# Kernel optimization log

Measured on AMD Instinct MI355X. Metric: run time of the kernel, lower is better.

## Reference

```python
import jax, jax.numpy as jnp
import numpy as np

N = 8192
EMB = 256
KDIM = 32
AR = 1024
UTYPE = 233
TEMP = 0.8


def setup_inputs() -> dict:
    key = jax.random.key(0)
    ks = jax.random.split(key, 16)
    s = 0.05
    f32 = jnp.float32
    inp = {
        'utype_mask': jax.random.uniform(ks[0], (UTYPE,), f32),
        'entity_mask': jnp.ones((N,), f32),
        'entity_encodings': jax.random.normal(ks[1], (N, EMB), f32),
        'autoregressive_encoding': jax.random.normal(ks[2], (AR,), f32),
        # func_embed: Linear(233,256)+ReLU
        'W_fe': jax.random.normal(ks[3], (EMB, UTYPE), f32) * s, 'b_fe': jnp.zeros((EMB,), f32),
        # entity_keys: Conv1d(256,32,1) == pointwise linear
        'W_k': jax.random.normal(ks[4], (KDIM, EMB), f32) * s, 'b_k': jnp.zeros((KDIM,), f32),
        # argenc[0]: Linear(1024,256)
        'W_a0': jax.random.normal(ks[5], (EMB, AR), f32) * s, 'b_a0': jnp.zeros((EMB,), f32),
        # argenc[1]: ReLU -> Linear(256,32) -> ReLU
        'W_a1': jax.random.normal(ks[6], (KDIM, EMB), f32) * s, 'b_a1': jnp.zeros((KDIM,), f32),
        # LSTM(64,32) gates (forget, input-sigmoid, input-tanh, output) + shared LayerNorm(32)
        'W_f': jax.random.normal(ks[7], (KDIM, 2 * KDIM), f32) * s, 'b_f': jnp.zeros((KDIM,), f32),
        'W_i0': jax.random.normal(ks[8], (KDIM, 2 * KDIM), f32) * s, 'b_i0': jnp.zeros((KDIM,), f32),
        'W_i1': jax.random.normal(ks[9], (KDIM, 2 * KDIM), f32) * s, 'b_i1': jnp.zeros((KDIM,), f32),
        'W_o': jax.random.normal(ks[10], (KDIM, 2 * KDIM), f32) * s, 'b_o': jnp.zeros((KDIM,), f32),
        'ln_g': jnp.ones((KDIM,), f32), 'ln_b': jnp.zeros((KDIM,), f32),
        # argenc[3]: Linear(32,1024)+ReLU
        'W_a3': jax.random.normal(ks[11], (AR, KDIM), f32) * s, 'b_a3': jnp.zeros((AR,), f32),
        'self_unit_ct': 64,
    }
    return inp


def reference(utype_mask, entity_mask, entity_encodings, autoregressive_encoding,
              W_fe, b_fe, W_k, b_k, W_a0, b_a0, W_a1, b_a1,
              W_f, b_f, W_i0, b_i0, W_i1, b_i1, W_o, b_o, ln_g, ln_b,
              W_a3, b_a3, self_unit_ct):
    n = entity_encodings.shape[0]
    steps = min(64, int(self_unit_ct))

    def ln(x):  # shared LayerNorm(32), torch eps=1e-5, biased var
        m = x.mean()
        v = ((x - m) ** 2).mean()
        return (x - m) * jax.lax.rsqrt(v + 1e-5) * ln_g + ln_b

    def lstm(x, h):
        forget = ln(jax.nn.sigmoid(W_f @ x + b_f))
        remember = ln(jax.nn.sigmoid(W_i0 @ x + b_i0) * jnp.tanh(W_i1 @ x + b_i1))
        new_h = remember + forget * h
        out = jnp.tanh(new_h) * ln(jax.nn.sigmoid(W_o @ x + b_o))
        return out, new_h

    func_embed = jax.nn.relu(W_fe @ utype_mask + b_fe)          # (256,)
    keys = W_k @ entity_encodings.T + b_k[:, None]               # (32, N)

    def step(carry, _):
        q, h, mask, ar, sel, done = carry
        active = jnp.logical_not(done)
        i0 = W_a0 @ ar + b_a0 + func_embed                       # (256,)
        i1 = jax.nn.relu(W_a1 @ jax.nn.relu(i0) + b_a1)          # (32,)
        qn, hn = lstm(jnp.concatenate([i1, q]), h)
        sig = jax.nn.sigmoid(qn @ keys)                          # (N,)
        v = jnp.nan_to_num(jnp.exp(jnp.log(sig) / TEMP))
        ssum = v.sum()
        valid = ssum != 0
        soft = jnp.where(valid, v / jnp.where(valid, ssum, 1.0), 0.0)
        row = jnp.where(active & valid, soft, 0.0)
        pick = jnp.argmax(soft)                                  # deterministic stand-in for multinomial sample
        hit = active & valid & (mask[pick] != 0)
        selection = keys[:, pick]
        centered = selection - selection.mean()
        nan_free = jnp.logical_not(jnp.any(jnp.isnan(centered)))
        mask = jnp.where(hit, mask.at[pick].set(0.0), mask)
        sel = jnp.where(hit, sel.at[pick].set(1.0), sel)
        ar = jnp.where(hit & nan_free, ar + jax.nn.relu(W_a3 @ centered + b_a3), ar)
        done = done | (hit & jnp.logical_not(nan_free))          # emulates break
        q = jnp.where(active, qn, q)
        h = jnp.where(active, hn, h)
        return (q, h, mask, ar, sel, done), row

    init = (jnp.zeros((KDIM,), jnp.float32), jnp.zeros((KDIM,), jnp.float32),
            entity_mask, autoregressive_encoding,
            jnp.zeros((n,), jnp.float32), jnp.array(False))
    (_, _, _, ar_out, sel_out, _), rows = jax.lax.scan(step, init, None, length=steps)
    unit_logits = jnp.zeros((n, n), jnp.float32).at[:steps].set(rows)
    return unit_logits, sel_out, ar_out
```

## Files before the change

kernel.cpp:

```cpp
#include <hip/hip_runtime.h>
#include <math.h>


typedef float v4f __attribute__((ext_vector_type(4)));
typedef unsigned long long ull;

#define N_ENT 8192
#define EMB   256
#define KD    32
#define ARD   1024
#define UT    233
#define NSCAN 32
#define NZERO 224
#define NBLK  256

#define WS_KEYS 0
#define WS_C0   262144
#define WS_PAIR 262400
#define PR_RI0W  0
#define PR_CRI0  512
#define PR_CPART 577
#define PR_KMAX  641
#define PR_SACC  705
#define NPAIRS   737

struct Params {
  const float *um, *emask, *enc, *arin, *W_fe, *b_fe, *W_k, *b_k,
              *W_a0, *b_a0, *W_a1, *b_a1, *W_f, *b_f, *W_i0, *b_i0,
              *W_i1, *b_i1, *W_o, *b_o, *ln_g, *ln_b, *W_a3, *b_a3;
  const int* ct;
  float* out;
  float* wsf;
  int*   wsi;
};

__device__ __forceinline__ ull ld_pair(ull* p_) {
  return __hip_atomic_load(p_, __ATOMIC_RELAXED, __HIP_MEMORY_SCOPE_AGENT);
}
__device__ __forceinline__ void st_pair(ull* p_, ull v) {
  __hip_atomic_store(p_, v, __ATOMIC_RELAXED, __HIP_MEMORY_SCOPE_AGENT);
}
__device__ __forceinline__ void wait_ctr(ull* c, ull target) {
  int guard = 0;
  while (__hip_atomic_load(c, __ATOMIC_RELAXED, __HIP_MEMORY_SCOPE_AGENT) < target) {
    __builtin_amdgcn_s_sleep(1);
    if (++guard > (1 << 20)) break;
  }
}

__global__ __launch_bounds__(256) void k_init(Params p) {
  __shared__ float enc_s[32 * 260];
  __shared__ float um_s[UT];
  const int tid = threadIdx.x, bid = blockIdx.x;
  float* keys = p.wsf + WS_KEYS;

  if (bid == 0 && tid < UT) um_s[tid] = p.um[tid];
  if (bid == 3) {
    ull* pr = (ull*)(p.wsf + WS_PAIR);
    for (int i = tid; i < NPAIRS; i += 256) pr[i] = 0ull;
  }

  const int j0 = bid * 32;
  #pragma unroll
  for (int i = 0; i < 8; ++i) {
    int idx = i * 256 + tid;
    int row = idx >> 6, c4 = idx & 63;
    v4f v = *(const v4f*)(p.enc + (size_t)(j0 + row) * EMB + c4 * 4);
    *(v4f*)&enc_s[row * 260 + c4 * 4] = v;
  }
  __syncthreads();
  {
    const int jl = tid >> 3, kg = tid & 7;
    float acc[4];
    #pragma unroll
    for (int kk = 0; kk < 4; ++kk) acc[kk] = p.b_k[kg * 4 + kk];
    for (int e4 = 0; e4 < 64; ++e4) {
      v4f x = *(const v4f*)&enc_s[jl * 260 + e4 * 4];
      #pragma unroll
      for (int kk = 0; kk < 4; ++kk) {
        v4f w = *(const v4f*)(p.W_k + (size_t)(kg * 4 + kk) * EMB + e4 * 4);
        acc[kk] += x.x * w.x + x.y * w.y + x.z * w.z + x.w * w.w;
      }
    }
    const int j = j0 + jl;
    #pragma unroll
    for (int kk = 0; kk < 4; ++kk) keys[(size_t)(kg * 4 + kk) * N_ENT + j] = acc[kk];
  }
  if (bid == 0) {
    float a = p.b_fe[tid];
    const float* wr = p.W_fe + (size_t)tid * UT;
    for (int u = 0; u < UT; ++u) a += wr[u] * um_s[u];
    p.wsf[WS_C0 + tid] = fmaxf(a, 0.f) + p.b_a0[tid];
  }
}

__global__ __launch_bounds__(256, 1) void k_scan(Params p) {
  const int tid = threadIdx.x, bid = blockIdx.x;
  int ctv = p.ct[0];
  const int steps = ctv < 0 ? 0 : (ctv > 64 ? 64 : ctv);
  const size_t NN = (size_t)N_ENT * N_ENT;

  if (bid >= NSCAN) {
    v4f z = (v4f){0.f, 0.f, 0.f, 0.f};
    v4f* o4 = (v4f*)p.out;
    const size_t tot = NN / 4;
    for (size_t i = (size_t)steps * (N_ENT / 4) + (size_t)(bid - NSCAN) * 256 + tid;
         i < tot; i += (size_t)NZERO * 256)
      __builtin_nontemporal_store(z, o4 + i);
    return;
  }

  __shared__ float ar_s[32 * 33];
  __shared__ float ri0_s[8 * 33];
  __shared__ unsigned maskb[256], selb[256];
  __shared__ float x_i1[32], q_s[32], h_s[32], qnf[32];
  __shared__ float garr[128], fog[32], rem[32], og[32], cent[32];
  __shared__ float b_a1s[32], gb_s[128], lng_s[32], lnb_s[32], c0own[8];
  __shared__ float reds[4], rmaxs[4];
  __shared__ int   ridxs[4];
  __shared__ float ssum_s;
  __shared__ int   upd_s, done_s;

  ull*   pairb = (ull*)(p.wsf + WS_PAIR);
  ull*   ri0w  = pairb + PR_RI0W;
  ull*   cri0  = pairb + PR_CRI0;
  ull*   cpart = pairb + PR_CPART;
  ull*   kmaxp = pairb + PR_KMAX;
  float* saccp = (float*)(pairb + PR_SACC);
  const float* keys = p.wsf + WS_KEYS;

  for (int i = tid; i < ARD; i += 256) ar_s[(i >> 5) * 33 + (i & 31)] = p.arin[i];
  {
    unsigned mb = 0u;
    const float* em = p.emask + (size_t)tid * 32;
    #pragma unroll
    for (int j = 0; j < 32; ++j) mb |= (em[j] != 0.f) ? (1u << j) : 0u;
    maskb[tid] = mb; selb[tid] = 0u;
  }
  if (tid < 32) {
    b_a1s[tid] = p.b_a1[tid];
    lng_s[tid] = p.ln_g[tid]; lnb_s[tid] = p.ln_b[tid];
    q_s[tid] = 0.f; h_s[tid] = 0.f; qnf[tid] = 0.f; x_i1[tid] = 0.f;
  }
  if (tid < 128) {
    const int g = tid >> 5, r = tid & 31;
    const float* bg = (g == 0) ? p.b_f : (g == 1) ? p.b_i0 : (g == 2) ? p.b_i1 : p.b_o;
    gb_s[tid] = bg[r];
  }
  if (tid < 8) c0own[tid] = p.wsf[WS_C0 + bid * 8 + tid];
  if (tid == 0) done_s = 0;

  v4f w0[8];
  { const float* s = p.W_a0 + (size_t)(bid * 8 + (tid >> 5)) * ARD + (tid & 31) * 32;
    #pragma unroll
    for (int i = 0; i < 8; ++i) w0[i] = ((const v4f*)s)[i]; }
  v4f w1[8];
  { const float* s = p.W_a1 + (size_t)(tid >> 3) * EMB + (tid & 7) * 32;
    #pragma unroll
    for (int i = 0; i < 8; ++i) w1[i] = ((const v4f*)s)[i]; }
  v4f wg[8];
  { const int rowg = tid >> 1, g = rowg >> 5, r = rowg & 31, half = tid & 1;
    const float* W = (g == 0) ? p.W_f : (g == 1) ? p.W_i0 : (g == 2) ? p.W_i1 : p.W_o;
    const float* s = W + r * 64 + half * 32;
    #pragma unroll
    for (int i = 0; i < 8; ++i) wg[i] = ((const v4f*)s)[i]; }
  float kc[32];
  { const int gcol = bid * 256 + tid;
    #pragma unroll
    for (int k = 0; k < 32; ++k) kc[k] = keys[(size_t)k * N_ENT + gcol]; }
  __syncthreads();

  auto produce = [&](int tt) {
    const int seg = tid & 31, rl = tid >> 5;
    const float* a = &ar_s[seg * 33];
    float pa = 0.f;
    #pragma unroll
    for (int i = 0; i < 8; ++i) {
      v4f av = *(const v4f*)(a + 4 * i);
      pa += w0[i].x * av.x + w0[i].y * av.y + w0[i].z * av.z + w0[i].w * av.w;
    }
    #pragma unroll
    for (int m = 16; m; m >>= 1) pa += __shfl_xor(pa, m);
    if (seg == 0)
      st_pair(&ri0w[(tt & 1) * 256 + bid * 8 + rl],
              (ull)__float_as_uint(fmaxf(pa + c0own[rl], 0.f)));
  };
  produce(0);
  __syncthreads();
  if (tid == 0)
    __hip_atomic_fetch_add(&cri0[0], 1ull, __ATOMIC_RELAXED, __HIP_MEMORY_SCOPE_AGENT);

  float v_reg = 0.f;
  for (int t = 0; t < steps; ++t) {
    if (tid == 0) wait_ctr(&cri0[t], (ull)NSCAN);
    __syncthreads();
    {
      ull u = ld_pair(&ri0w[(t & 1) * 256 + tid]);
      ri0_s[(tid >> 5) * 33 + (tid & 31)] = __uint_as_float((unsigned)u);
    }
    __syncthreads();
    const int act = (done_s == 0);
    {
      const int r = tid >> 3, s8 = tid & 7;
      float p1 = 0.f;
      #pragma unroll
      for (int i = 0; i < 8; ++i) {
        const float* xx = &ri0_s[s8 * 33 + 4 * i];
        p1 += w1[i].x * xx[0] + w1[i].y * xx[1] + w1[i].z * xx[2] + w1[i].w * xx[3];
      }
      #pragma unroll
      for (int m = 4; m; m >>= 1) p1 += __shfl_xor(p1, m);
      if (s8 == 0) x_i1[r] = fmaxf(p1 + b_a1s[r], 0.f);
    }
    __syncthreads();
    {
      const int rowg = tid >> 1, g = rowg >> 5, half = tid & 1;
      const float* xsrc = half ? q_s : x_i1;
      float pg = 0.f;
      #pragma unroll
      for (int i = 0; i < 8; ++i)
        pg += wg[i].x * xsrc[4 * i] + wg[i].y * xsrc[4 * i + 1] +
              wg[i].z * xsrc[4 * i + 2] + wg[i].w * xsrc[4 * i + 3];
      pg += __shfl_xor(pg, 1);
      if (!half) {
        pg += gb_s[rowg];
        garr[rowg] = (g == 2) ? tanhf(pg) : 1.f / (1.f + __expf(-pg));
      }
    }
    __syncthreads();
    {
      const int w = tid >> 6, k = tid & 63;
      if (w < 3 && k < 32) {
        float a = (w == 0) ? garr[k] : (w == 1) ? garr[32 + k] * garr[64 + k] : garr[96 + k];
        float s = a;
        #pragma unroll
        for (int m = 16; m; m >>= 1) s += __shfl_xor(s, m);
        const float mean = s * (1.f / 32.f);
        const float d = a - mean;
        float vv = d * d;
        #pragma unroll
        for (int m = 16; m; m >>= 1) vv += __shfl_xor(vv, m);
        vv *= (1.f / 32.f);
        const float y = d * rsqrtf(vv + 1e-5f) * lng_s[k] + lnb_s[k];
        if (w == 0) fog[k] = y; else if (w == 1) rem[k] = y; else og[k] = y;
      }
    }
    __syncthreads();
    if (tid < 32) {
      const float nh = rem[tid] + fog[tid] * h_s[tid];
      const float qv = tanhf(nh) * og[tid];
      qnf[tid] = qv;
      if (act) { h_s[tid] = nh; q_s[tid] = qv; }
    }
    __syncthreads();

    {
      float dot = 0.f;
      #pragma unroll
      for (int k = 0; k < 32; ++k) dot += qnf[k] * kc[k];
      const float sig = 1.f / (1.f + __expf(-dot));
      const float v = __expf(__logf(sig) / 0.8f);
      v_reg = v;
      float sv = v, mv = v;
      int mi = (bid << 8) + tid;
      #pragma unroll
      for (int m = 32; m; m >>= 1) {
        sv += __shfl_xor(sv, m);
        const float ov = __shfl_xor(mv, m);
        const int oi = __shfl_xor(mi, m);
        if (ov > mv || (ov == mv && oi < mi)) { mv = ov; mi = oi; }
      }
      const int wv = tid >> 6;
      if ((tid & 63) == 0) { reds[wv] = sv; rmaxs[wv] = mv; ridxs[wv] = mi; }
    }
    __syncthreads();
    if (tid == 0) {
      float Sb = ((reds[0] + reds[1]) + reds[2]) + reds[3];
      float Mb = rmaxs[0]; int Ib = ridxs[0];
      #pragma unroll
      for (int i2 = 1; i2 < 4; ++i2)
        if (rmaxs[i2] > Mb || (rmaxs[i2] == Mb && ridxs[i2] < Ib)) { Mb = rmaxs[i2]; Ib = ridxs[i2]; }
      __hip_atomic_fetch_add(&saccp[t], Sb, __ATOMIC_RELAXED, __HIP_MEMORY_SCOPE_AGENT);
      const ull key = ((ull)__float_as_uint(Mb) << 32) | (ull)(0xFFFFFFFFu - (unsigned)Ib);
      __hip_atomic_fetch_max(&kmaxp[t], key, __ATOMIC_RELAXED, __HIP_MEMORY_SCOPE_AGENT);
      asm volatile("s_waitcnt vmcnt(0)" ::: "memory");
      __hip_atomic_fetch_add(&cpart[t], 1ull, __ATOMIC_RELAXED, __HIP_MEMORY_SCOPE_AGENT);
    }

    if (tid == 0) wait_ctr(&cpart[t], (ull)NSCAN);
    __syncthreads();
    if (tid < 32) {
      const float s = __hip_atomic_load(&saccp[t], __ATOMIC_RELAXED, __HIP_MEMORY_SCOPE_AGENT);
      const ull km = ld_pair(&kmaxp[t]);
      const int ii = (int)(0xFFFFFFFFu - (unsigned)(km & 0xFFFFFFFFull));
      const float kv = keys[(size_t)tid * N_ENT + ii];
      float mn = kv;
      #pragma unroll
      for (int mm = 16; mm; mm >>= 1) mn += __shfl_xor(mn, mm);
      mn *= (1.f / 32.f);
      const float cv = kv - mn;
      cent[tid] = cv;
      const unsigned long long bb = __ballot(cv != cv);
      if (tid == 0) {
        const int valid = (s != 0.f);
        const int nf = (bb == 0) ? 1 : 0;
        const unsigned mw = maskb[ii >> 5];
        const int hit = (act && valid && ((mw >> (ii & 31)) & 1)) ? 1 : 0;
        ssum_s = s;
        upd_s = (hit && nf) ? 1 : 0;
        if (hit) {
          maskb[ii >> 5] = mw & ~(1u << (ii & 31));
          selb[ii >> 5] |= (1u << (ii & 31));
          if (!nf) done_s = 1;
        }
      }
    }
    __syncthreads();
    {
      const float S = ssum_s;
      const float rowv = (act && (S != 0.f)) ? (v_reg / S) : 0.f;
      __builtin_nontemporal_store(rowv, p.out + (size_t)t * N_ENT + (bid << 8) + tid);
    }
    if (upd_s) {
      #pragma unroll
      for (int rr = 0; rr < 4; ++rr) {
        const int r = tid + rr * 256;
        const float* wr = p.W_a3 + (size_t)r * KD;
        float dl = p.b_a3[r];
        #pragma unroll
        for (int c4 = 0; c4 < 8; ++c4) {
          v4f wv4 = *(const v4f*)(wr + 4 * c4);
          dl += wv4.x * cent[4 * c4] + wv4.y * cent[4 * c4 + 1] +
                wv4.z * cent[4 * c4 + 2] + wv4.w * cent[4 * c4 + 3];
        }
        if (dl > 0.f) ar_s[(r >> 5) * 33 + (r & 31)] += dl;
      }
    }
    __syncthreads();
    produce(t + 1);
    __syncthreads();
    if (tid == 0)
      __hip_atomic_fetch_add(&cri0[t + 1], 1ull, __ATOMIC_RELAXED, __HIP_MEMORY_SCOPE_AGENT);
  }
  __syncthreads();

  if (bid == 0) {
    for (int i = tid; i < N_ENT; i += 256)
      p.out[NN + i] = ((selb[i >> 5] >> (i & 31)) & 1u) ? 1.f : 0.f;
  } else if (bid == 1) {
    for (int i = tid; i < ARD; i += 256)
      p.out[NN + N_ENT + i] = ar_s[(i >> 5) * 33 + (i & 31)];
  }
}

extern "C" void kernel_launch(void* const* d_in, const int* in_sizes, int n_in,
                              void* d_out, int out_size, void* d_ws, size_t ws_size,
                              hipStream_t stream) {
  (void)in_sizes; (void)n_in; (void)out_size; (void)ws_size;
  Params p;
  p.um    = (const float*)d_in[0];
  p.emask = (const float*)d_in[1];
  p.enc   = (const float*)d_in[2];
  p.arin  = (const float*)d_in[3];
  p.W_fe  = (const float*)d_in[4];
  p.b_fe  = (const float*)d_in[5];
  p.W_k   = (const float*)d_in[6];
  p.b_k   = (const float*)d_in[7];
  p.W_a0  = (const float*)d_in[8];
  p.b_a0  = (const float*)d_in[9];
  p.W_a1  = (const float*)d_in[10];
  p.b_a1  = (const float*)d_in[11];
  p.W_f   = (const float*)d_in[12];
  p.b_f   = (const float*)d_in[13];
  p.W_i0  = (const float*)d_in[14];
  p.b_i0  = (const float*)d_in[15];
  p.W_i1  = (const float*)d_in[16];
  p.b_i1  = (const float*)d_in[17];
  p.W_o   = (const float*)d_in[18];
  p.b_o   = (const float*)d_in[19];
  p.ln_g  = (const float*)d_in[20];
  p.ln_b  = (const float*)d_in[21];
  p.W_a3  = (const float*)d_in[22];
  p.b_a3  = (const float*)d_in[23];
  p.ct    = (const int*)d_in[24];
  p.out   = (float*)d_out;
  p.wsf   = (float*)d_ws;
  p.wsi   = (int*)d_ws;

  hipLaunchKernelGGL(k_init, dim3(NBLK), dim3(256), 0, stream, p);
  hipLaunchKernelGGL(k_scan, dim3(NBLK), dim3(256), 0, stream, p);
}
```

Measured before the change: 881.1 us.

## Replace global atomic reductions with tagged per-block records and lighter barriers

Each block now publishes its partial softmax sum, max and argmax as tagged 64-bit records instead of doing float atomic-add and atomic-max on shared global cells. Every block then gathers all 32 records and reduces them with wave shuffles. The ri0 buffer uses step tags instead of double-buffering, and the counters are padded to separate cache lines. __syncthreads is replaced by a raw lgkmcnt wait plus s_barrier. The aim is to cut cross-block atomic contention and barrier overhead on the serial 64-step critical path, at the cost of tag-polling loops and weaker memory-ordering guarantees from the custom barrier.

```diff
diff --git a/kernel.cpp b/kernel.cpp
--- a/kernel.cpp
+++ b/kernel.cpp
@@ -18,11 +18,10 @@
 #define WS_C0   262144
 #define WS_PAIR 262400
 #define PR_RI0W  0
-#define PR_CRI0  512
-#define PR_CPART 577
-#define PR_KMAX  641
-#define PR_SACC  705
-#define NPAIRS   737
+#define PR_PART  256
+#define PR_CRI0  384
+#define PR_CPART 904
+#define NPAIRS   1416
 
 struct Params {
   const float *um, *emask, *enc, *arin, *W_fe, *b_fe, *W_k, *b_k,
@@ -40,12 +39,24 @@
 __device__ __forceinline__ void st_pair(ull* p_, ull v) {
   __hip_atomic_store(p_, v, __ATOMIC_RELAXED, __HIP_MEMORY_SCOPE_AGENT);
 }
+__device__ __forceinline__ ull packf(float v, unsigned tag) {
+  return ((ull)tag << 32) | (ull)__float_as_uint(v);
+}
+__device__ __forceinline__ ull packi(int v, unsigned tag) {
+  return ((ull)tag << 32) | (ull)(unsigned)v;
+}
+__device__ __forceinline__ unsigned ptag(ull u) { return (unsigned)(u >> 32); }
+__device__ __forceinline__ float pvalf(ull u) { return __uint_as_float((unsigned)u); }
 __device__ __forceinline__ void wait_ctr(ull* c, ull target) {
   int guard = 0;
   while (__hip_atomic_load(c, __ATOMIC_RELAXED, __HIP_MEMORY_SCOPE_AGENT) < target) {
     __builtin_amdgcn_s_sleep(1);
     if (++guard > (1 << 20)) break;
   }
+}
+
+__device__ __forceinline__ void bar_lds() {
+  asm volatile("s_waitcnt lgkmcnt(0)\n\ts_barrier" ::: "memory");
 }
 
 __global__ __launch_bounds__(256) void k_init(Params p) {
@@ -121,12 +132,11 @@
   __shared__ float ssum_s;
   __shared__ int   upd_s, done_s;
 
-  ull*   pairb = (ull*)(p.wsf + WS_PAIR);
-  ull*   ri0w  = pairb + PR_RI0W;
-  ull*   cri0  = pairb + PR_CRI0;
-  ull*   cpart = pairb + PR_CPART;
-  ull*   kmaxp = pairb + PR_KMAX;
-  float* saccp = (float*)(pairb + PR_SACC);
+  ull* pairb = (ull*)(p.wsf + WS_PAIR);
+  ull* ri0w  = pairb + PR_RI0W;
+  ull* partp = pairb + PR_PART;
+  ull* cri0  = pairb + PR_CRI0;
+  ull* cpart = pairb + PR_CPART;
   const float* keys = p.wsf + WS_KEYS;
 
   for (int i = tid; i < ARD; i += 256) ar_s[(i >> 5) * 33 + (i & 31)] = p.arin[i];
@@ -182,23 +192,31 @@
     #pragma unroll
     for (int m = 16; m; m >>= 1) pa += __shfl_xor(pa, m);
     if (seg == 0)
-      st_pair(&ri0w[(tt & 1) * 256 + bid * 8 + rl],
-              (ull)__float_as_uint(fmaxf(pa + c0own[rl], 0.f)));
+      st_pair(&ri0w[bid * 8 + rl],
+              packf(fmaxf(pa + c0own[rl], 0.f), (unsigned)(tt + 1)));
   };
   produce(0);
-  __syncthreads();
+  bar_lds();
   if (tid == 0)
     __hip_atomic_fetch_add(&cri0[0], 1ull, __ATOMIC_RELAXED, __HIP_MEMORY_SCOPE_AGENT);
 
   float v_reg = 0.f;
   for (int t = 0; t < steps; ++t) {
-    if (tid == 0) wait_ctr(&cri0[t], (ull)NSCAN);
-    __syncthreads();
-    {
-      ull u = ld_pair(&ri0w[(t & 1) * 256 + tid]);
-      ri0_s[(tid >> 5) * 33 + (tid & 31)] = __uint_as_float((unsigned)u);
-    }
-    __syncthreads();
+    const unsigned tg = (unsigned)(t + 1);
+
+    if (tid == 0) wait_ctr(&cri0[t * 8], (ull)NSCAN);
+    bar_lds();
+    {
+      ull u = ld_pair(&ri0w[tid]);
+      int guard = 0;
+      while (ptag(u) != tg) {
+        if (++guard > (1 << 20)) break;
+        __builtin_amdgcn_s_sleep(1);
+        u = ld_pair(&ri0w[tid]);
+      }
+      ri0_s[(tid >> 5) * 33 + (tid & 31)] = pvalf(u);
+    }
+    bar_lds();
     const int act = (done_s == 0);
     {
       const int r = tid >> 3, s8 = tid & 7;
@@ -212,7 +230,7 @@
       for (int m = 4; m; m >>= 1) p1 += __shfl_xor(p1, m);
       if (s8 == 0) x_i1[r] = fmaxf(p1 + b_a1s[r], 0.f);
     }
-    __syncthreads();
+    bar_lds();
     {
       const int rowg = tid >> 1, g = rowg >> 5, half = tid & 1;
       const float* xsrc = half ? q_s : x_i1;
@@ -227,7 +245,7 @@
         garr[rowg] = (g == 2) ? tanhf(pg) : 1.f / (1.f + __expf(-pg));
       }
     }
-    __syncthreads();
+    bar_lds();
     {
       const int w = tid >> 6, k = tid & 63;
       if (w < 3 && k < 32) {
@@ -245,14 +263,14 @@
         if (w == 0) fog[k] = y; else if (w == 1) rem[k] = y; else og[k] = y;
       }
     }
-    __syncthreads();
+    bar_lds();
     if (tid < 32) {
       const float nh = rem[tid] + fog[tid] * h_s[tid];
       const float qv = tanhf(nh) * og[tid];
       qnf[tid] = qv;
       if (act) { h_s[tid] = nh; q_s[tid] = qv; }
     }
-    __syncthreads();
+    bar_lds();
 
     {
       float dot = 0.f;
@@ -273,26 +291,39 @@
       const int wv = tid >> 6;
       if ((tid & 63) == 0) { reds[wv] = sv; rmaxs[wv] = mv; ridxs[wv] = mi; }
     }
-    __syncthreads();
+    bar_lds();
     if (tid == 0) {
       float Sb = ((reds[0] + reds[1]) + reds[2]) + reds[3];
       float Mb = rmaxs[0]; int Ib = ridxs[0];
       #pragma unroll
       for (int i2 = 1; i2 < 4; ++i2)
         if (rmaxs[i2] > Mb || (rmaxs[i2] == Mb && ridxs[i2] < Ib)) { Mb = rmaxs[i2]; Ib = ridxs[i2]; }
-      __hip_atomic_fetch_add(&saccp[t], Sb, __ATOMIC_RELAXED, __HIP_MEMORY_SCOPE_AGENT);
-      const ull key = ((ull)__float_as_uint(Mb) << 32) | (ull)(0xFFFFFFFFu - (unsigned)Ib);
-      __hip_atomic_fetch_max(&kmaxp[t], key, __ATOMIC_RELAXED, __HIP_MEMORY_SCOPE_AGENT);
-      asm volatile("s_waitcnt vmcnt(0)" ::: "memory");
-      __hip_atomic_fetch_add(&cpart[t], 1ull, __ATOMIC_RELAXED, __HIP_MEMORY_SCOPE_AGENT);
-    }
-
-    if (tid == 0) wait_ctr(&cpart[t], (ull)NSCAN);
-    __syncthreads();
+      ull* rec = &partp[bid * 4];
+      st_pair(&rec[0], packf(Sb, tg));
+      st_pair(&rec[1], packf(Mb, tg));
+      st_pair(&rec[2], packi(Ib, tg));
+      __hip_atomic_fetch_add(&cpart[t * 8], 1ull, __ATOMIC_RELAXED, __HIP_MEMORY_SCOPE_AGENT);
+    }
+
     if (tid < 32) {
-      const float s = __hip_atomic_load(&saccp[t], __ATOMIC_RELAXED, __HIP_MEMORY_SCOPE_AGENT);
-      const ull km = ld_pair(&kmaxp[t]);
-      const int ii = (int)(0xFFFFFFFFu - (unsigned)(km & 0xFFFFFFFFull));
+      if (tid == 0) wait_ctr(&cpart[t * 8], (ull)NSCAN);
+      ull* rec = &partp[tid * 4];
+      ull u0 = ld_pair(&rec[0]), u1 = ld_pair(&rec[1]), u2 = ld_pair(&rec[2]);
+      int guard = 0;
+      while (ptag(u0) != tg || ptag(u1) != tg || ptag(u2) != tg) {
+        if (++guard > (1 << 20)) break;
+        __builtin_amdgcn_s_sleep(1);
+        u0 = ld_pair(&rec[0]); u1 = ld_pair(&rec[1]); u2 = ld_pair(&rec[2]);
+      }
+      float s = pvalf(u0), m = pvalf(u1);
+      int ii = (int)(unsigned)u2;
+      #pragma unroll
+      for (int mm = 16; mm; mm >>= 1) {
+        s += __shfl_xor(s, mm);
+        const float om = __shfl_xor(m, mm);
+        const int oi = __shfl_xor(ii, mm);
+        if (om > m || (om == m && oi < ii)) { m = om; ii = oi; }
+      }
       const float kv = keys[(size_t)tid * N_ENT + ii];
       float mn = kv;
       #pragma unroll
@@ -315,7 +346,7 @@
         }
       }
     }
-    __syncthreads();
+    bar_lds();
     {
       const float S = ssum_s;
       const float rowv = (act && (S != 0.f)) ? (v_reg / S) : 0.f;
@@ -336,11 +367,11 @@
         if (dl > 0.f) ar_s[(r >> 5) * 33 + (r & 31)] += dl;
       }
     }
-    __syncthreads();
+    bar_lds();
     produce(t + 1);
-    __syncthreads();
+    bar_lds();
     if (tid == 0)
-      __hip_atomic_fetch_add(&cri0[t + 1], 1ull, __ATOMIC_RELAXED, __HIP_MEMORY_SCOPE_AGENT);
+      __hip_atomic_fetch_add(&cri0[(t + 1) * 8], 1ull, __ATOMIC_RELAXED, __HIP_MEMORY_SCOPE_AGENT);
   }
   __syncthreads();
 
```

Measured after the change: 895.2 us. About the same (+1.6%).

## Skip cross-block AR recompute when autoregressive encoding is unchanged

Applied to the files above, without the earlier changes.

The per-step recompute of the first argenc layer and its grid-wide counter barrier now runs only when the previous step actually updated the autoregressive encoding (a hit with no NaN). Otherwise the cached x_i1 is reused. Steps after a done flag write zeros and skip all work. This removes a global synchronization and a matvec from steps where the input is unchanged, but it relies on every block reaching the same upd_s and done decisions so the epoch counters stay consistent.

```diff
diff --git a/kernel.cpp b/kernel.cpp
--- a/kernel.cpp
+++ b/kernel.cpp
@@ -170,7 +170,7 @@
     for (int k = 0; k < 32; ++k) kc[k] = keys[(size_t)k * N_ENT + gcol]; }
   __syncthreads();
 
-  auto produce = [&](int tt) {
+  auto produce = [&](int e) {
     const int seg = tid & 31, rl = tid >> 5;
     const float* a = &ar_s[seg * 33];
     float pa = 0.f;
@@ -182,7 +182,7 @@
     #pragma unroll
     for (int m = 16; m; m >>= 1) pa += __shfl_xor(pa, m);
     if (seg == 0)
-      st_pair(&ri0w[(tt & 1) * 256 + bid * 8 + rl],
+      st_pair(&ri0w[(e & 1) * 256 + bid * 8 + rl],
               (ull)__float_as_uint(fmaxf(pa + c0own[rl], 0.f)));
   };
   produce(0);
@@ -190,29 +190,41 @@
   if (tid == 0)
     __hip_atomic_fetch_add(&cri0[0], 1ull, __ATOMIC_RELAXED, __HIP_MEMORY_SCOPE_AGENT);
 
+  int ep = 0;
+  int pend = 1;
   float v_reg = 0.f;
   for (int t = 0; t < steps; ++t) {
-    if (tid == 0) wait_ctr(&cri0[t], (ull)NSCAN);
-    __syncthreads();
-    {
-      ull u = ld_pair(&ri0w[(t & 1) * 256 + tid]);
-      ri0_s[(tid >> 5) * 33 + (tid & 31)] = __uint_as_float((unsigned)u);
-    }
-    __syncthreads();
     const int act = (done_s == 0);
-    {
-      const int r = tid >> 3, s8 = tid & 7;
-      float p1 = 0.f;
-      #pragma unroll
-      for (int i = 0; i < 8; ++i) {
-        const float* xx = &ri0_s[s8 * 33 + 4 * i];
-        p1 += w1[i].x * xx[0] + w1[i].y * xx[1] + w1[i].z * xx[2] + w1[i].w * xx[3];
-      }
-      #pragma unroll
-      for (int m = 4; m; m >>= 1) p1 += __shfl_xor(p1, m);
-      if (s8 == 0) x_i1[r] = fmaxf(p1 + b_a1s[r], 0.f);
-    }
-    __syncthreads();
+
+    if (!act) {
+      __builtin_nontemporal_store(0.f, p.out + (size_t)t * N_ENT + (bid << 8) + tid);
+      continue;
+    }
+
+    if (pend) {
+      if (tid == 0) wait_ctr(&cri0[ep], (ull)NSCAN);
+      __syncthreads();
+      {
+        ull u = ld_pair(&ri0w[(ep & 1) * 256 + tid]);
+        ri0_s[(tid >> 5) * 33 + (tid & 31)] = __uint_as_float((unsigned)u);
+      }
+      __syncthreads();
+      {
+        const int r = tid >> 3, s8 = tid & 7;
+        float p1 = 0.f;
+        #pragma unroll
+        for (int i = 0; i < 8; ++i) {
+          const float* xx = &ri0_s[s8 * 33 + 4 * i];
+          p1 += w1[i].x * xx[0] + w1[i].y * xx[1] + w1[i].z * xx[2] + w1[i].w * xx[3];
+        }
+        #pragma unroll
+        for (int m = 4; m; m >>= 1) p1 += __shfl_xor(p1, m);
+        if (s8 == 0) x_i1[r] = fmaxf(p1 + b_a1s[r], 0.f);
+      }
+      __syncthreads();
+      pend = 0;
+    }
+
     {
       const int rowg = tid >> 1, g = rowg >> 5, half = tid & 1;
       const float* xsrc = half ? q_s : x_i1;
@@ -250,7 +262,7 @@
       const float nh = rem[tid] + fog[tid] * h_s[tid];
       const float qv = tanhf(nh) * og[tid];
       qnf[tid] = qv;
-      if (act) { h_s[tid] = nh; q_s[tid] = qv; }
+      h_s[tid] = nh; q_s[tid] = qv;
     }
     __syncthreads();
 
@@ -305,7 +317,7 @@
         const int valid = (s != 0.f);
         const int nf = (bb == 0) ? 1 : 0;
         const unsigned mw = maskb[ii >> 5];
-        const int hit = (act && valid && ((mw >> (ii & 31)) & 1)) ? 1 : 0;
+        const int hit = (valid && ((mw >> (ii & 31)) & 1)) ? 1 : 0;
         ssum_s = s;
         upd_s = (hit && nf) ? 1 : 0;
         if (hit) {
@@ -318,7 +330,7 @@
     __syncthreads();
     {
       const float S = ssum_s;
-      const float rowv = (act && (S != 0.f)) ? (v_reg / S) : 0.f;
+      const float rowv = (S != 0.f) ? (v_reg / S) : 0.f;
       __builtin_nontemporal_store(rowv, p.out + (size_t)t * N_ENT + (bid << 8) + tid);
     }
     if (upd_s) {
@@ -337,10 +349,14 @@
       }
     }
     __syncthreads();
-    produce(t + 1);
-    __syncthreads();
-    if (tid == 0)
-      __hip_atomic_fetch_add(&cri0[t + 1], 1ull, __ATOMIC_RELAXED, __HIP_MEMORY_SCOPE_AGENT);
+    if (upd_s) {
+      ep += 1;
+      produce(ep);
+      __syncthreads();
+      if (tid == 0)
+        __hip_atomic_fetch_add(&cri0[ep], 1ull, __ATOMIC_RELAXED, __HIP_MEMORY_SCOPE_AGENT);
+      pend = 1;
+    }
   }
   __syncthreads();
 
```

New measurement: 744.4 us. 1.18x faster.
